# Kernel optimization log

Measured on AMD Instinct MI355X. Metric: run time of the kernel, lower is better.

Reference implementation:

```python
import jax, jax.numpy as jnp
import numpy as np

N_NODES = 50000
N_EDGES = 800000
D_IN = 64
D_HID = 256
BN_EPS = 1e-5


def setup_inputs() -> dict:
    key = jax.random.key(0)
    ks = jax.random.split(key, 8)
    s = 1.0 / np.sqrt(D_IN)
    sg = 1.0 / np.sqrt(D_HID)
    return {
        "xs": jax.random.normal(ks[0], (N_NODES, D_IN), jnp.float32),
        "edge_index": jax.random.randint(ks[1], (2, N_EDGES), 0, N_NODES, jnp.int64),
        "W_gcn": jax.random.normal(ks[2], (D_IN, D_HID), jnp.float32) * s,
        "b_gcn": jnp.zeros((D_HID,), jnp.float32),
        "W_lin": jax.random.normal(ks[3], (D_IN, D_HID), jnp.float32) * s,
        "b_lin": jnp.zeros((D_HID,), jnp.float32),
        "W_gate": jax.random.normal(ks[4], (D_HID, D_HID), jnp.float32) * sg,
        "b_gate": jnp.zeros((D_HID,), jnp.float32),
        "bn_gamma": jnp.ones((D_HID,), jnp.float32),
        "bn_beta": jnp.zeros((D_HID,), jnp.float32),
    }


def reference(xs, edge_index, W_gcn, b_gcn, W_lin, b_lin, W_gate, b_gate, bn_gamma, bn_beta):
    N = xs.shape[0]
    # --- GCNConv: add self loops, symmetric normalization D^-1/2 (A+I) D^-1/2 ---
    loops = jnp.arange(N, dtype=edge_index.dtype)
    src = jnp.concatenate([edge_index[0], loops])  # message sources
    dst = jnp.concatenate([edge_index[1], loops])  # aggregation targets
    deg = jax.ops.segment_sum(jnp.ones(src.shape, jnp.float32), dst, num_segments=N)
    dinv = jax.lax.rsqrt(jnp.maximum(deg, 1.0))  # deg >= 1 due to self loops
    norm = dinv[src] * dinv[dst]                 # [E+N]
    h = xs @ W_gcn                               # [N, D_HID]
    z = jax.ops.segment_sum(h[src] * norm[:, None], dst, num_segments=N) + b_gcn
    z = jnp.tanh(z)
    # --- gating + linear residual ---
    g = jax.nn.sigmoid(z @ W_gate + b_gate)
    xl = xs @ W_lin + b_lin
    out = jax.nn.relu((1.0 - g) * xl + g * z)
    # --- BatchNorm over nodes (training-mode batch statistics) ---
    mu = out.mean(axis=0)
    var = out.var(axis=0)
    out = (out - mu) * jax.lax.rsqrt(var + BN_EPS) * bn_gamma + bn_beta
    # dropout is identity in eval mode
    return out
```

## Files before the change

kernel.cpp:

```cpp
#include <hip/hip_runtime.h>
#include <math.h>

#define NN 50000
#define NE 800000
#define D_IN 64
#define D_HID 256
#define BN_EPS 1e-5f
#define ZSTR 264

typedef __attribute__((ext_vector_type(8))) short short8;
typedef __attribute__((ext_vector_type(4))) float f32x4;

static __device__ __forceinline__ unsigned short f2bf(float f) {
    unsigned int u = __builtin_bit_cast(unsigned int, f);
    u += 0x7FFFu + ((u >> 16) & 1u);
    return (unsigned short)(u >> 16);
}
static __device__ __forceinline__ float bf2f(unsigned short s) {
    unsigned int u = ((unsigned int)s) << 16;
    return __builtin_bit_cast(float, u);
}
static __device__ __forceinline__ float fast_sigmoid(float x) {
    return __builtin_amdgcn_rcpf(1.0f + __expf(-x));
}
static __device__ __forceinline__ float fast_tanh(float x) {
    return 1.0f - 2.0f * __builtin_amdgcn_rcpf(__expf(2.0f * x) + 1.0f);
}

static __device__ __forceinline__ long a_addr(int i, int k) {
    return ((long)((i >> 4) * 2 + (k >> 5)) << 9) + ((((k >> 3) & 3) * 16 + (i & 15)) << 3) + (k & 7);
}

__global__ __launch_bounds__(256) void k_pre(const float* __restrict__ W_gcn,
                      const float* __restrict__ W_lin, const float* __restrict__ W_gate,
                      unsigned short* __restrict__ Wp_gcn, unsigned short* __restrict__ Wp_lin,
                      unsigned short* __restrict__ Wp_gate,
                      const int* __restrict__ eidx, int* __restrict__ cnt, int E) {
    int idx = blockIdx.x * blockDim.x + threadIdx.x;
    if (idx < 98304) {
        const float* W;
        unsigned short* Wp;
        int KC, o;
        if (idx < 16384)      { W = W_gcn;  Wp = Wp_gcn;  KC = 2; o = idx; }
        else if (idx < 32768) { W = W_lin;  Wp = Wp_lin;  KC = 2; o = idx - 16384; }
        else                  { W = W_gate; Wp = Wp_gate; KC = 8; o = idx - 32768; }
        int j = o & 7;
        int lane = (o >> 3) & 63;
        int rest = o >> 9;
        int kc = rest % KC;
        int ct = rest / KC;
        int col = ct * 16 + (lane & 15);
        int k = kc * 32 + (lane >> 4) * 8 + j;
        Wp[o] = f2bf(W[k * D_HID + col]);
    }
    if (idx * 4 < E) {
        int4 d = *(const int4*)(eidx + E + idx * 4);
        atomicAdd(&cnt[d.x], 1);
        atomicAdd(&cnt[d.y], 1);
        atomicAdd(&cnt[d.z], 1);
        atomicAdd(&cnt[d.w], 1);
    }
}

__global__ __launch_bounds__(256) void k_scanprep(const float* __restrict__ xs,
                           const int* __restrict__ cnt,
                           int* __restrict__ offs, int* __restrict__ cursor,
                           float* __restrict__ dinv, unsigned short* __restrict__ xscaled,
                           unsigned short* __restrict__ xs_p, int* __restrict__ gtotal, int n) {
    int t = threadIdx.x;
    int b = blockIdx.x;
    int nb = (n + 255) >> 8;
    if (b < nb) {
        __shared__ int s[256];
        __shared__ int sbase;
        int i = b * 256 + t;
        int v = (i < n) ? cnt[i] : 0;
        s[t] = v;
        __syncthreads();
        for (int d = 1; d < 256; d <<= 1) {
            int t2 = (t >= d) ? s[t - d] : 0;
            __syncthreads();
            s[t] += t2;
            __syncthreads();
        }
        int incl = s[t];
        if (t == 255) sbase = atomicAdd(gtotal, incl);
        __syncthreads();
        if (i < n) {
            int o = sbase + incl - v;
            offs[i] = o;
            cursor[i] = o;
        }
    }
    int idx = b * 256 + t;
    if (idx >= n * 8) {
        if (idx < n * 8 + 8) {
            short8 zv = (short8){0, 0, 0, 0, 0, 0, 0, 0};
            *(short8*)(xscaled + (long)n * D_IN + (idx - n * 8) * 8) = zv;
        }
        return;
    }
    int i = idx >> 3;
    int sub = idx & 7;
    float dv = rsqrtf(1.0f + (float)cnt[i]);
    if (sub == 0) dinv[i] = dv;
    const float* p = xs + (long)i * D_IN + sub * 8;
    float4 f0 = *(const float4*)p;
    float4 f1 = *(const float4*)(p + 4);
    float vals[8] = {f0.x, f0.y, f0.z, f0.w, f1.x, f1.y, f1.z, f1.w};
    short8 xsc, xsb;
#pragma unroll
    for (int j = 0; j < 8; j++) {
        xsc[j] = (short)f2bf(vals[j] * dv);
        xsb[j] = (short)f2bf(vals[j]);
    }
    *(short8*)(xscaled + (long)i * D_IN + sub * 8) = xsc;
    *(short8*)(xs_p + a_addr(i, sub * 8)) = xsb;
}

__global__ __launch_bounds__(256) void k_scatter(const int* __restrict__ eidx,
                          int* __restrict__ cursor,
                          unsigned short* __restrict__ csr_src, int E) {
    int e4 = blockIdx.x * blockDim.x + threadIdx.x;
    if (e4 * 4 >= E) return;
    int4 s = *(const int4*)(eidx + e4 * 4);
    int4 d = *(const int4*)(eidx + E + e4 * 4);
    csr_src[atomicAdd(&cursor[d.x], 1)] = (unsigned short)s.x;
    csr_src[atomicAdd(&cursor[d.y], 1)] = (unsigned short)s.y;
    csr_src[atomicAdd(&cursor[d.z], 1)] = (unsigned short)s.z;
    csr_src[atomicAdd(&cursor[d.w], 1)] = (unsigned short)s.w;
}

__global__ __launch_bounds__(256) void k_gather(const unsigned short* __restrict__ csr_src,
                                                const int* __restrict__ offs,
                                                const int* __restrict__ cnt,
                                                const unsigned short* __restrict__ xscaled,
                                                const float* __restrict__ dinv,
                                                unsigned short* __restrict__ agg_p, int n) {
    int wv = threadIdx.x >> 6;
    int lane = threadIdx.x & 63;
    int sub = lane & 7;
    int grp = lane >> 3;
    int i = blockIdx.x * 4 + wv;
    if (i >= n) return;
    int start = offs[i];
    int c = cnt[i];
    float acc[8];
#pragma unroll
    for (int j = 0; j < 8; j++) acc[j] = 0.f;
    for (int base = 0; base < c; base += 64) {
        int m = c - base;
        m = m < 64 ? m : 64;
        int idxv = (lane < m) ? (int)csr_src[start + base + lane] : 0;
        int tmax = (m + 7) >> 3;
        for (int t = 0; t < tmax; t++) {
            int e = t * 8 + grp;
            int rowv = __shfl(idxv, e);
            int row = (e < m) ? rowv : n;
            short8 v = *(const short8*)(xscaled + (long)row * D_IN + sub * 8);
#pragma unroll
            for (int j = 0; j < 8; j++) acc[j] += bf2f((unsigned short)v[j]);
        }
    }
#pragma unroll
    for (int d = 8; d <= 32; d <<= 1)
#pragma unroll
        for (int j = 0; j < 8; j++) acc[j] += __shfl_xor(acc[j], d);
    if (grp == 0) {
        float dv = dinv[i];
        short8 sv = *(const short8*)(xscaled + (long)i * D_IN + sub * 8);
        short8 o;
#pragma unroll
        for (int j = 0; j < 8; j++)
            o[j] = (short)f2bf((acc[j] + bf2f((unsigned short)sv[j])) * dv);
        *(short8*)(agg_p + a_addr(i, sub * 8)) = o;
    }
}

__global__ __launch_bounds__(256) void k_fused(const unsigned short* __restrict__ agg_p,
                        const unsigned short* __restrict__ xs_p,
                        const unsigned short* __restrict__ Wp_gcn,
                        const unsigned short* __restrict__ Wp_lin,
                        const unsigned short* __restrict__ Wp_gate,
                        const float* __restrict__ b_gcn,
                        const float* __restrict__ bg,
                        const float* __restrict__ bl,
                        unsigned short* __restrict__ out_pre,
                        float* __restrict__ colsum,
                        float* __restrict__ colsumsq, int n) {
    __shared__ unsigned short z_lds[64 * ZSTR];

    int tid = threadIdx.x;
    int wv = tid >> 6;
    int lane = tid & 63;
    int l15 = lane & 15;
    int quad = lane >> 4;
    int row0 = blockIdx.x * 64;
    int rt0 = blockIdx.x * 4;

    {
        short8 wg[2][4];
#pragma unroll
        for (int kc = 0; kc < 2; kc++)
#pragma unroll
            for (int tn = 0; tn < 4; tn++)
                wg[kc][tn] = *(const short8*)(Wp_gcn + ((long)((wv * 4 + tn) * 2 + kc) << 9) + lane * 8);
        float bias[4];
#pragma unroll
        for (int tn = 0; tn < 4; tn++) bias[tn] = b_gcn[wv * 64 + tn * 16 + l15];
#pragma unroll
        for (int r = 0; r < 4; r++) {
            f32x4 accz[4];
#pragma unroll
            for (int c = 0; c < 4; c++) accz[c] = (f32x4){0.f, 0.f, 0.f, 0.f};
#pragma unroll
            for (int kc = 0; kc < 2; kc++) {
                short8 af = *(const short8*)(agg_p + ((long)((rt0 + r) * 2 + kc) << 9) + lane * 8);
#pragma unroll
                for (int tn = 0; tn < 4; tn++)
                    accz[tn] = __builtin_amdgcn_mfma_f32_16x16x32_bf16(af, wg[kc][tn], accz[tn], 0, 0, 0);
            }
#pragma unroll
            for (int tn = 0; tn < 4; tn++) {
                int col = wv * 64 + tn * 16 + l15;
#pragma unroll
                for (int r2 = 0; r2 < 4; r2++)
                    z_lds[(r * 16 + quad * 4 + r2) * ZSTR + col] = f2bf(fast_tanh(accz[tn][r2] + bias[tn]));
            }
        }
    }
    __syncthreads();

    uint2 o_pk[4][4];
    float ls[4] = {0.f, 0.f, 0.f, 0.f};
    float lsq[4] = {0.f, 0.f, 0.f, 0.f};
    float bgc[4], blc[4];
#pragma unroll
    for (int tn = 0; tn < 4; tn++) {
        int col = wv * 64 + tn * 16 + l15;
        bgc[tn] = bg[col];
        blc[tn] = bl[col];
    }
#pragma unroll
    for (int r = 0; r < 4; r++) {
        f32x4 accl[4];
#pragma unroll
        for (int c = 0; c < 4; c++) accl[c] = (f32x4){0.f, 0.f, 0.f, 0.f};
#pragma unroll
        for (int kc = 0; kc < 2; kc++) {
            short8 af = *(const short8*)(xs_p + ((long)((rt0 + r) * 2 + kc) << 9) + lane * 8);
#pragma unroll
            for (int tn = 0; tn < 4; tn++) {
                short8 wl = *(const short8*)(Wp_lin + ((long)((wv * 4 + tn) * 2 + kc) << 9) + lane * 8);
                accl[tn] = __builtin_amdgcn_mfma_f32_16x16x32_bf16(af, wl, accl[tn], 0, 0, 0);
            }
        }
        f32x4 acc1[4];
#pragma unroll
        for (int c = 0; c < 4; c++) acc1[c] = (f32x4){0.f, 0.f, 0.f, 0.f};
#pragma unroll
        for (int kc = 0; kc < 8; kc++) {
            short8 af = *(const short8*)(&z_lds[(r * 16 + l15) * ZSTR + kc * 32 + quad * 8]);
#pragma unroll
            for (int tn = 0; tn < 4; tn++) {
                short8 bfr = *(const short8*)(Wp_gate + ((long)((wv * 4 + tn) * 8 + kc) << 9) + lane * 8);
                acc1[tn] = __builtin_amdgcn_mfma_f32_16x16x32_bf16(af, bfr, acc1[tn], 0, 0, 0);
            }
        }
#pragma unroll
        for (int tn = 0; tn < 4; tn++) {
            int col = wv * 64 + tn * 16 + l15;
            unsigned short op[4];
#pragma unroll
            for (int r2 = 0; r2 < 4; r2++) {
                int rl = r * 16 + quad * 4 + r2;
                int row = row0 + rl;
                float g = fast_sigmoid(acc1[tn][r2] + bgc[tn]);
                float zv = bf2f(z_lds[rl * ZSTR + col]);
                float xv = accl[tn][r2] + blc[tn];
                float o = fmaxf((1.f - g) * xv + g * zv, 0.f);
                op[r2] = f2bf(o);
                if (row < n) {
                    ls[tn] += o;
                    lsq[tn] += o * o;
                }
            }
            o_pk[r][tn].x = (unsigned int)op[0] | ((unsigned int)op[1] << 16);
            o_pk[r][tn].y = (unsigned int)op[2] | ((unsigned int)op[3] << 16);
        }
    }
    __syncthreads();

#pragma unroll
    for (int r = 0; r < 4; r++)
#pragma unroll
        for (int tn = 0; tn < 4; tn++) {
            int col = wv * 64 + tn * 16 + l15;
            int rl = r * 16 + quad * 4;
            *(unsigned int*)(&z_lds[(rl + 0) * ZSTR + col]) ;
            z_lds[(rl + 0) * ZSTR + col] = (unsigned short)(o_pk[r][tn].x & 0xFFFF);
            z_lds[(rl + 1) * ZSTR + col] = (unsigned short)(o_pk[r][tn].x >> 16);
            z_lds[(rl + 2) * ZSTR + col] = (unsigned short)(o_pk[r][tn].y & 0xFFFF);
            z_lds[(rl + 3) * ZSTR + col] = (unsigned short)(o_pk[r][tn].y >> 16);
        }
    __syncthreads();

#pragma unroll
    for (int it = 0; it < 8; it++) {
        int g = it * 2048 + tid * 8;
        int row = g >> 8;
        int col = g & 255;
        short8 v = *(const short8*)(&z_lds[row * ZSTR + col]);
        *(short8*)(out_pre + (long)(row0 + row) * D_HID + col) = v;
    }

#pragma unroll
    for (int tn = 0; tn < 4; tn++) {
        float s = ls[tn];
        float q = lsq[tn];
        s += __shfl_xor(s, 16);
        s += __shfl_xor(s, 32);
        q += __shfl_xor(q, 16);
        q += __shfl_xor(q, 32);
        if (quad == 0) {
            int col = wv * 64 + tn * 16 + l15;
            atomicAdd(&colsum[col], s);
            atomicAdd(&colsumsq[col], q);
        }
    }
}

__global__ __launch_bounds__(256) void k_bn_apply(const unsigned short* __restrict__ op,
                           float* __restrict__ out,
                           const float* __restrict__ colsum, const float* __restrict__ colsumsq,
                           const float* __restrict__ gamma, const float* __restrict__ beta,
                           int n, int total8) {
    int i8 = blockIdx.x * blockDim.x + threadIdx.x;
    if (i8 >= total8) return;
    long idx = (long)i8 * 8;
    short8 p = *(const short8*)(op + idx);
    int c = (int)(idx & (D_HID - 1));
    float inv_n = 1.0f / (float)n;
    float vo[8];
#pragma unroll
    for (int j = 0; j < 8; j++) {
        float mu = colsum[c + j] * inv_n;
        float var = colsumsq[c + j] * inv_n - mu * mu;
        float sc = gamma[c + j] * rsqrtf(var + BN_EPS);
        vo[j] = bf2f((unsigned short)p[j]) * sc + (beta[c + j] - mu * sc);
    }
    float4 v0 = {vo[0], vo[1], vo[2], vo[3]};
    float4 v1 = {vo[4], vo[5], vo[6], vo[7]};
    *(float4*)(out + idx) = v0;
    *(float4*)(out + idx + 4) = v1;
}

extern "C" void kernel_launch(void* const* d_in, const int* in_sizes, int n_in,
                              void* d_out, int out_size, void* d_ws, size_t ws_size,
                              hipStream_t stream) {
    const float* xs     = (const float*)d_in[0];
    const int*   eidx   = (const int*)d_in[1];
    const float* W_gcn  = (const float*)d_in[2];
    const float* b_gcn  = (const float*)d_in[3];
    const float* W_lin  = (const float*)d_in[4];
    const float* b_lin  = (const float*)d_in[5];
    const float* W_gate = (const float*)d_in[6];
    const float* b_gate = (const float*)d_in[7];
    const float* gamma  = (const float*)d_in[8];
    const float* beta   = (const float*)d_in[9];
    float* out = (float*)d_out;

    const int n = in_sizes[0] / D_IN;
    const int E = in_sizes[1] / 2;
    const int npad = (n + 63) & ~63;

    char* ws = (char*)d_ws;
    size_t off = 0;
    auto alloc = [&](size_t bytes) {
        char* p = ws + off;
        off += (bytes + 511) & ~(size_t)511;
        return p;
    };
    size_t zero_begin = off;
    int*            cnt      = (int*)alloc((size_t)n * 4);
    float*          colsum   = (float*)alloc(D_HID * 4);
    float*          colsumsq = (float*)alloc(D_HID * 4);
    int*            gtotal   = (int*)alloc(4);
    size_t zero_end = off;
    int*            offs     = (int*)alloc((size_t)n * 4);
    int*            cursor   = (int*)alloc((size_t)n * 4);
    unsigned short* csr_src  = (unsigned short*)alloc((size_t)(E + 64) * 2);
    float*          dinv     = (float*)alloc((size_t)n * 4);
    unsigned short* xscaled  = (unsigned short*)alloc((size_t)(n + 1) * D_IN * 2);
    unsigned short* xs_p     = (unsigned short*)alloc((size_t)npad * D_IN * 2);
    unsigned short* agg_p    = (unsigned short*)alloc((size_t)npad * D_IN * 2);
    unsigned short* out_pre  = (unsigned short*)alloc((size_t)npad * D_HID * 2);
    unsigned short* Wp_gcn   = (unsigned short*)alloc((size_t)D_IN * D_HID * 2);
    unsigned short* Wp_lin   = (unsigned short*)alloc((size_t)D_IN * D_HID * 2);
    unsigned short* Wp_gate  = (unsigned short*)alloc((size_t)D_HID * D_HID * 2);
    (void)ws_size;

    const int B = 256;

    hipMemsetAsync(ws + zero_begin, 0, zero_end - zero_begin, stream);
    k_pre<<<(E / 4 + B - 1) / B, B, 0, stream>>>(W_gcn, W_lin, W_gate, Wp_gcn, Wp_lin, Wp_gate,
                                                 eidx, cnt, E);
    k_scanprep<<<(n * 8 + 8 + B - 1) / B, B, 0, stream>>>(xs, cnt, offs, cursor, dinv,
                                                          xscaled, xs_p, gtotal, n);
    k_scatter<<<(E / 4 + B - 1) / B, B, 0, stream>>>(eidx, cursor, csr_src, E);
    k_gather<<<(n + 3) / 4, B, 0, stream>>>(csr_src, offs, cnt, xscaled, dinv, agg_p, n);
    k_fused<<<npad / 64, B, 0, stream>>>(agg_p, xs_p, Wp_gcn, Wp_lin, Wp_gate,
                                         b_gcn, b_gate, b_lin, out_pre, colsum, colsumsq, n);
    {
        int total8 = n * D_HID / 8;
        k_bn_apply<<<(total8 + B - 1) / B, B, 0, stream>>>(out_pre, out, colsum, colsumsq,
                                                           gamma, beta, n, total8);
    }
}
```

Measured before the change: 265.1 us.

## Move BN column statistics to separate kernel and reorder gate GEMM loops

```diff
diff --git a/kernel.cpp b/kernel.cpp
--- a/kernel.cpp
+++ b/kernel.cpp
@@ -7,6 +7,7 @@
 #define D_HID 256
 #define BN_EPS 1e-5f
 #define ZSTR 264
+#define SB 128
 
 typedef __attribute__((ext_vector_type(8))) short short8;
 typedef __attribute__((ext_vector_type(4))) float f32x4;
@@ -186,8 +187,7 @@
                         const float* __restrict__ bg,
                         const float* __restrict__ bl,
                         unsigned short* __restrict__ out_pre,
-                        float* __restrict__ colsum,
-                        float* __restrict__ colsumsq, int n) {
+                        int n) {
     __shared__ unsigned short z_lds[64 * ZSTR];
 
     int tid = threadIdx.x;
@@ -197,6 +197,7 @@
     int quad = lane >> 4;
     int row0 = blockIdx.x * 64;
     int rt0 = blockIdx.x * 4;
+    (void)row0;
 
     {
         short8 wg[2][4];
@@ -232,8 +233,6 @@
     __syncthreads();
 
     uint2 o_pk[4][4];
-    float ls[4] = {0.f, 0.f, 0.f, 0.f};
-    float lsq[4] = {0.f, 0.f, 0.f, 0.f};
     float bgc[4], blc[4];
 #pragma unroll
     for (int tn = 0; tn < 4; tn++) {
@@ -242,51 +241,58 @@
         blc[tn] = bl[col];
     }
 #pragma unroll
-    for (int r = 0; r < 4; r++) {
-        f32x4 accl[4];
-#pragma unroll
-        for (int c = 0; c < 4; c++) accl[c] = (f32x4){0.f, 0.f, 0.f, 0.f};
+    for (int tnp = 0; tnp < 2; tnp++) {
+        f32x4 accl[4][2];
+#pragma unroll
+        for (int r = 0; r < 4; r++)
+#pragma unroll
+            for (int h = 0; h < 2; h++) accl[r][h] = (f32x4){0.f, 0.f, 0.f, 0.f};
 #pragma unroll
         for (int kc = 0; kc < 2; kc++) {
-            short8 af = *(const short8*)(xs_p + ((long)((rt0 + r) * 2 + kc) << 9) + lane * 8);
-#pragma unroll
-            for (int tn = 0; tn < 4; tn++) {
-                short8 wl = *(const short8*)(Wp_lin + ((long)((wv * 4 + tn) * 2 + kc) << 9) + lane * 8);
-                accl[tn] = __builtin_amdgcn_mfma_f32_16x16x32_bf16(af, wl, accl[tn], 0, 0, 0);
+            short8 wl0 = *(const short8*)(Wp_lin + ((long)((wv * 4 + tnp * 2 + 0) * 2 + kc) << 9) + lane * 8);
+            short8 wl1 = *(const short8*)(Wp_lin + ((long)((wv * 4 + tnp * 2 + 1) * 2 + kc) << 9) + lane * 8);
+#pragma unroll
+            for (int r = 0; r < 4; r++) {
+                short8 af = *(const short8*)(xs_p + ((long)((rt0 + r) * 2 + kc) << 9) + lane * 8);
+                accl[r][0] = __builtin_amdgcn_mfma_f32_16x16x32_bf16(af, wl0, accl[r][0], 0, 0, 0);
+                accl[r][1] = __builtin_amdgcn_mfma_f32_16x16x32_bf16(af, wl1, accl[r][1], 0, 0, 0);
             }
         }
-        f32x4 acc1[4];
-#pragma unroll
-        for (int c = 0; c < 4; c++) acc1[c] = (f32x4){0.f, 0.f, 0.f, 0.f};
+        f32x4 acc1[4][2];
+#pragma unroll
+        for (int r = 0; r < 4; r++)
+#pragma unroll
+            for (int h = 0; h < 2; h++) acc1[r][h] = (f32x4){0.f, 0.f, 0.f, 0.f};
 #pragma unroll
         for (int kc = 0; kc < 8; kc++) {
-            short8 af = *(const short8*)(&z_lds[(r * 16 + l15) * ZSTR + kc * 32 + quad * 8]);
-#pragma unroll
-            for (int tn = 0; tn < 4; tn++) {
-                short8 bfr = *(const short8*)(Wp_gate + ((long)((wv * 4 + tn) * 8 + kc) << 9) + lane * 8);
-                acc1[tn] = __builtin_amdgcn_mfma_f32_16x16x32_bf16(af, bfr, acc1[tn], 0, 0, 0);
+            short8 w0 = *(const short8*)(Wp_gate + ((long)((wv * 4 + tnp * 2 + 0) * 8 + kc) << 9) + lane * 8);
+            short8 w1 = *(const short8*)(Wp_gate + ((long)((wv * 4 + tnp * 2 + 1) * 8 + kc) << 9) + lane * 8);
+#pragma unroll
+            for (int r = 0; r < 4; r++) {
+                short8 af = *(const short8*)(&z_lds[(r * 16 + l15) * ZSTR + kc * 32 + quad * 8]);
+                acc1[r][0] = __builtin_amdgcn_mfma_f32_16x16x32_bf16(af, w0, acc1[r][0], 0, 0, 0);
+                acc1[r][1] = __builtin_amdgcn_mfma_f32_16x16x32_bf16(af, w1, acc1[r][1], 0, 0, 0);
             }
         }
 #pragma unroll
-        for (int tn = 0; tn < 4; tn++) {
+        for (int h = 0; h < 2; h++) {
+            int tn = tnp * 2 + h;
             int col = wv * 64 + tn * 16 + l15;
-            unsigned short op[4];
-#pragma unroll
-            for (int r2 = 0; r2 < 4; r2++) {
-                int rl = r * 16 + quad * 4 + r2;
-                int row = row0 + rl;
-                float g = fast_sigmoid(acc1[tn][r2] + bgc[tn]);
-                float zv = bf2f(z_lds[rl * ZSTR + col]);
-                float xv = accl[tn][r2] + blc[tn];
-                float o = fmaxf((1.f - g) * xv + g * zv, 0.f);
-                op[r2] = f2bf(o);
-                if (row < n) {
-                    ls[tn] += o;
-                    lsq[tn] += o * o;
+#pragma unroll
+            for (int r = 0; r < 4; r++) {
+                unsigned short op4[4];
+#pragma unroll
+                for (int r2 = 0; r2 < 4; r2++) {
+                    int rl = r * 16 + quad * 4 + r2;
+                    float g = fast_sigmoid(acc1[r][h][r2] + bgc[tn]);
+                    float zv = bf2f(z_lds[rl * ZSTR + col]);
+                    float xv = accl[r][h][r2] + blc[tn];
+                    float o = fmaxf((1.f - g) * xv + g * zv, 0.f);
+                    op4[r2] = f2bf(o);
                 }
+                o_pk[r][tn].x = (unsigned int)op4[0] | ((unsigned int)op4[1] << 16);
+                o_pk[r][tn].y = (unsigned int)op4[2] | ((unsigned int)op4[3] << 16);
             }
-            o_pk[r][tn].x = (unsigned int)op[0] | ((unsigned int)op[1] << 16);
-            o_pk[r][tn].y = (unsigned int)op[2] | ((unsigned int)op[3] << 16);
         }
     }
     __syncthreads();
@@ -297,7 +303,6 @@
         for (int tn = 0; tn < 4; tn++) {
             int col = wv * 64 + tn * 16 + l15;
             int rl = r * 16 + quad * 4;
-            *(unsigned int*)(&z_lds[(rl + 0) * ZSTR + col]) ;
             z_lds[(rl + 0) * ZSTR + col] = (unsigned short)(o_pk[r][tn].x & 0xFFFF);
             z_lds[(rl + 1) * ZSTR + col] = (unsigned short)(o_pk[r][tn].x >> 16);
             z_lds[(rl + 2) * ZSTR + col] = (unsigned short)(o_pk[r][tn].y & 0xFFFF);
@@ -311,21 +316,52 @@
         int row = g >> 8;
         int col = g & 255;
         short8 v = *(const short8*)(&z_lds[row * ZSTR + col]);
-        *(short8*)(out_pre + (long)(row0 + row) * D_HID + col) = v;
-    }
-
-#pragma unroll
-    for (int tn = 0; tn < 4; tn++) {
-        float s = ls[tn];
-        float q = lsq[tn];
-        s += __shfl_xor(s, 16);
-        s += __shfl_xor(s, 32);
-        q += __shfl_xor(q, 16);
-        q += __shfl_xor(q, 32);
-        if (quad == 0) {
-            int col = wv * 64 + tn * 16 + l15;
-            atomicAdd(&colsum[col], s);
-            atomicAdd(&colsumsq[col], q);
+        *(short8*)(out_pre + (long)(blockIdx.x * 64 + row) * D_HID + col) = v;
+    }
+    (void)n;
+}
+
+__global__ __launch_bounds__(256) void k_stats(const unsigned short* __restrict__ op,
+                        float* __restrict__ colsum, float* __restrict__ colsumsq, int n) {
+    __shared__ float reds[4][32][8];
+    __shared__ float redq[4][32][8];
+    int tid = threadIdx.x;
+    int wv = tid >> 6;
+    int lane = tid & 63;
+    int cg = tid & 31;
+    int rb = tid >> 5;
+    float ls[8], lq[8];
+#pragma unroll
+    for (int j = 0; j < 8; j++) { ls[j] = 0.f; lq[j] = 0.f; }
+    for (int row = blockIdx.x * 8 + rb; row < n; row += SB * 8) {
+        short8 v = *(const short8*)(op + (long)row * D_HID + cg * 8);
+#pragma unroll
+        for (int j = 0; j < 8; j++) {
+            float f = bf2f((unsigned short)v[j]);
+            ls[j] += f;
+            lq[j] += f * f;
+        }
+    }
+#pragma unroll
+    for (int j = 0; j < 8; j++) {
+        ls[j] += __shfl_xor(ls[j], 32);
+        lq[j] += __shfl_xor(lq[j], 32);
+    }
+    if (lane < 32) {
+#pragma unroll
+        for (int j = 0; j < 8; j++) {
+            reds[wv][cg][j] = ls[j];
+            redq[wv][cg][j] = lq[j];
+        }
+    }
+    __syncthreads();
+    if (wv == 0 && lane < 32) {
+#pragma unroll
+        for (int j = 0; j < 8; j++) {
+            float s = reds[0][cg][j] + reds[1][cg][j] + reds[2][cg][j] + reds[3][cg][j];
+            float q = redq[0][cg][j] + redq[1][cg][j] + redq[2][cg][j] + redq[3][cg][j];
+            atomicAdd(&colsum[cg * 8 + j], s);
+            atomicAdd(&colsumsq[cg * 8 + j], q);
         }
     }
 }
@@ -410,7 +446,8 @@
     k_scatter<<<(E / 4 + B - 1) / B, B, 0, stream>>>(eidx, cursor, csr_src, E);
     k_gather<<<(n + 3) / 4, B, 0, stream>>>(csr_src, offs, cnt, xscaled, dinv, agg_p, n);
     k_fused<<<npad / 64, B, 0, stream>>>(agg_p, xs_p, Wp_gcn, Wp_lin, Wp_gate,
-                                         b_gcn, b_gate, b_lin, out_pre, colsum, colsumsq, n);
+                                         b_gcn, b_gate, b_lin, out_pre, n);
+    k_stats<<<SB, B, 0, stream>>>(out_pre, colsum, colsumsq, n);
     {
         int total8 = n * D_HID / 8;
         k_bn_apply<<<(total8 + B - 1) / B, B, 0, stream>>>(out_pre, out, colsum, colsumsq,
```

New measurement: 289.0 us. 9.0% more time.
